# Performance work log

Hardware: AMD Instinct MI355X
Metric: run time of the kernel (lower is better)

Reference implementation:

```python
import jax, jax.numpy as jnp
import numpy as np

D_MODEL = 1024
N_HEADS = 16
HEAD_DIM = D_MODEL // N_HEADS


def setup_inputs() -> dict:
    key = jax.random.key(0)
    k_x, k_q, k_k, k_v = jax.random.split(key, 4)
    B, S = 2, 2048
    x = jax.random.normal(k_x, (B, S, D_MODEL), dtype=jnp.float32)
    # nn.Linear weights stored as [out, in]; we apply x @ W.T
    scale = 1.0 / np.sqrt(D_MODEL)
    W_q = jax.random.uniform(k_q, (D_MODEL, D_MODEL), jnp.float32, -scale, scale)
    W_k = jax.random.uniform(k_k, (D_MODEL, D_MODEL), jnp.float32, -scale, scale)
    W_v = jax.random.uniform(k_v, (D_MODEL, D_MODEL), jnp.float32, -scale, scale)
    return {"x": x, "W_q": W_q, "W_k": W_k, "W_v": W_v}


def reference(x, W_q, W_k, W_v):
    B, S, D = x.shape
    H, Hd = N_HEADS, HEAD_DIM
    # QKV projections (Linear with no bias): x @ W.T
    Q = (x @ W_q.T).reshape(B, S, H, Hd).transpose(0, 2, 1, 3)  # [B,H,S,Hd]
    K = (x @ W_k.T).reshape(B, S, H, Hd).transpose(0, 2, 1, 3)
    V = (x @ W_v.T).reshape(B, S, H, Hd).transpose(0, 2, 1, 3)
    scores = jnp.einsum("bhqd,bhkd->bhqk", Q, K) / jnp.sqrt(jnp.float32(Hd))
    attn = jax.nn.softmax(scores, axis=-1)
    out = jnp.einsum("bhqk,bhkd->bhqd", attn, V)  # [B,H,S,Hd]
    return out.transpose(0, 2, 1, 3).reshape(B, S, H * Hd)
```

## Files before the change

### kernel.cpp

```cpp
#include <hip/hip_runtime.h>
#include <stdint.h>


typedef __bf16 bf16x8 __attribute__((ext_vector_type(8)));
typedef __bf16 bf16x4 __attribute__((ext_vector_type(4)));
typedef float  f32x4  __attribute__((ext_vector_type(4)));
typedef float  f32x16 __attribute__((ext_vector_type(16)));

#define D_MODEL 1024
#define SEQ     2048
#define NHEAD   16
#define HDIM    64
#define BS      4096

__device__ __forceinline__ void load_lds16(const void* g, void* lds) {
  __builtin_amdgcn_global_load_lds(
      (__attribute__((address_space(1))) void*)(uintptr_t)g,
      (__attribute__((address_space(3))) void*)(uintptr_t)lds,
      16, 0, 0);
}

#define NX4 1048576
#define NW4 262144
__global__ void cvt_all(const float* __restrict__ x,  const float* __restrict__ wq,
                        const float* __restrict__ wk, const float* __restrict__ wv,
                        __bf16* __restrict__ xb,  __bf16* __restrict__ wqb,
                        __bf16* __restrict__ wkb, __bf16* __restrict__ wvb) {
  int i = blockIdx.x * blockDim.x + threadIdx.x;
  const float* in; __bf16* out; int j;
  if (i < NX4)                { in = x;  out = xb;  j = i; }
  else if (i < NX4 + NW4)     { in = wq; out = wqb; j = i - NX4; }
  else if (i < NX4 + 2*NW4)   { in = wk; out = wkb; j = i - NX4 - NW4; }
  else                        { in = wv; out = wvb; j = i - NX4 - 2*NW4; }
  float4 v = ((const float4*)in)[j];
  bf16x4 o;
  o[0] = (__bf16)v.x; o[1] = (__bf16)v.y;
  o[2] = (__bf16)v.z; o[3] = (__bf16)v.w;
  ((bf16x4*)out)[j] = o;
}

__global__ __launch_bounds__(256) void qkv_gemm(
    const __bf16* __restrict__ X,
    const __bf16* __restrict__ Wq, const __bf16* __restrict__ Wk,
    const __bf16* __restrict__ Wv,
    __bf16* __restrict__ Qb, __bf16* __restrict__ Kb, __bf16* __restrict__ Vt) {
  __shared__ __bf16 As[128 * 32];
  __shared__ __bf16 Bs[128 * 32];

  const __bf16* W = (blockIdx.z == 0) ? Wq : (blockIdx.z == 1) ? Wk : Wv;

  const int t    = threadIdx.x;
  const int wv   = t >> 6;
  const int lane = t & 63;
  const int l15  = lane & 15;
  const int quad = lane >> 4;
  const int m0   = blockIdx.y * 128;
  const int n0   = blockIdx.x * 128;
  const int wm   = (wv >> 1) * 64;
  const int wn   = (wv & 1) * 64;

  f32x4 acc[4][4] = {};

  for (int it = 0; it < 32; ++it) {
    const int k0 = it * 32;
#pragma unroll
    for (int p = 0; p < 2; ++p) {
      const int c   = p * 256 + t;
      const int row = c >> 2;
      const int ko  = (c & 3) * 8;
      const unsigned lb = (unsigned)((p * 256 + wv * 64) * 16);
      load_lds16(X + (size_t)(m0 + row) * D_MODEL + k0 + ko, (char*)As + lb);
      load_lds16(W + (size_t)(n0 + row) * D_MODEL + k0 + ko, (char*)Bs + lb);
    }
    __syncthreads();

    bf16x8 af[4], bfb[4];
#pragma unroll
    for (int i = 0; i < 4; ++i)
      af[i] = *(const bf16x8*)&As[(wm + i * 16 + l15) * 32 + quad * 8];
#pragma unroll
    for (int j = 0; j < 4; ++j)
      bfb[j] = *(const bf16x8*)&Bs[(wn + j * 16 + l15) * 32 + quad * 8];
#pragma unroll
    for (int i = 0; i < 4; ++i)
#pragma unroll
      for (int j = 0; j < 4; ++j)
        acc[i][j] = __builtin_amdgcn_mfma_f32_16x16x32_bf16(af[i], bfb[j],
                                                            acc[i][j], 0, 0, 0);
    __syncthreads();
  }

  if (blockIdx.z != 2) {
    __bf16* Out = (blockIdx.z == 0) ? Qb : Kb;
    const float qs = (blockIdx.z == 0) ? 0.125f : 1.0f;
#pragma unroll
    for (int i = 0; i < 4; ++i) {
      const int rg = m0 + wm + i * 16 + quad * 4;
#pragma unroll
      for (int j = 0; j < 4; ++j) {
        const int cg = n0 + wn + j * 16 + l15;
#pragma unroll
        for (int r = 0; r < 4; ++r)
          Out[(size_t)(rg + r) * D_MODEL + cg] = (__bf16)(acc[i][j][r] * qs);
      }
    }
  } else {
#pragma unroll
    for (int i = 0; i < 4; ++i) {
      const int mg = m0 + wm + i * 16 + quad * 4;
#pragma unroll
      for (int j = 0; j < 4; ++j) {
        const int ng = n0 + wn + j * 16 + l15;
        bf16x4 v;
#pragma unroll
        for (int r = 0; r < 4; ++r) v[r] = (__bf16)acc[i][j][r];
        *(bf16x4*)&Vt[(size_t)ng * BS + mg] = v;
      }
    }
  }
}

__global__ __launch_bounds__(256) void attn(
    const __bf16* __restrict__ Qb, const __bf16* __restrict__ Kb,
    const __bf16* __restrict__ Vt, float* __restrict__ out) {
  __shared__ __bf16 Ks[64 * 64];
  __shared__ __bf16 Vs[64 * 64];

  const int t    = threadIdx.x;
  const int wv   = t >> 6;
  const int lane = t & 63;
  const int l31  = lane & 31;
  const int half = lane >> 5;
  const int h    = blockIdx.y;
  const size_t bo = (size_t)blockIdx.z * SEQ;
  const int q0   = blockIdx.x * 128 + wv * 32;
  const int hd0  = h * HDIM;

  bf16x8 qf[4];
#pragma unroll
  for (int c = 0; c < 4; ++c)
    qf[c] = *(const bf16x8*)&Qb[(bo + q0 + l31) * D_MODEL + hd0 + c * 16 + half * 8];

  float lsum = 0.f;
  f32x16 o_acc[2] = {};

  for (int kt = 0; kt < SEQ / 64; ++kt) {
    const int n0 = kt * 64;
#pragma unroll
    for (int p = 0; p < 2; ++p) {
      const int c   = p * 256 + t;
      const int row = c >> 3;
      const int cc  = (c & 7) ^ (row & 7);
      const unsigned lb = (unsigned)((p * 256 + wv * 64) * 16);
      load_lds16(Kb + (bo + n0 + row) * D_MODEL + hd0 + cc * 8, (char*)Ks + lb);
      load_lds16(Vt + (size_t)(hd0 + row) * BS + bo + n0 + cc * 8, (char*)Vs + lb);
    }
    __syncthreads();

    f32x16 st[2];
#pragma unroll
    for (int ktile = 0; ktile < 2; ++ktile) {
      f32x16 acc = {};
      const int row = ktile * 32 + l31;
#pragma unroll
      for (int c = 0; c < 4; ++c) {
        const int pc = (2 * c + half) ^ (row & 7);
        bf16x8 kf = *(const bf16x8*)&Ks[(row * 8 + pc) * 8];
        acc = __builtin_amdgcn_mfma_f32_32x32x16_bf16(kf, qf[c], acc, 0, 0, 0);
      }
      st[ktile] = acc;
    }

    uint32_t pk[2][8];
#pragma unroll
    for (int ktile = 0; ktile < 2; ++ktile)
#pragma unroll
      for (int i = 0; i < 8; ++i) {
        float e0 = __expf(st[ktile][2 * i]);
        float e1 = __expf(st[ktile][2 * i + 1]);
        lsum += e0 + e1;
        union { bf16x4 v; uint32_t u[2]; } pp;
        pp.v[0] = (__bf16)e0; pp.v[1] = (__bf16)e1;
        pk[ktile][i] = pp.u[0];
      }

#pragma unroll
    for (int ktile = 0; ktile < 2; ++ktile)
#pragma unroll
      for (int kc = 0; kc < 2; ++kc) {
        auto r02 = __builtin_amdgcn_permlane32_swap(pk[ktile][kc * 4 + 0],
                                                    pk[ktile][kc * 4 + 2],
                                                    false, false);
        auto r13 = __builtin_amdgcn_permlane32_swap(pk[ktile][kc * 4 + 1],
                                                    pk[ktile][kc * 4 + 3],
                                                    false, false);
        union { uint32_t u[4]; bf16x8 v; } pf;
        pf.u[0] = r02[0]; pf.u[1] = r13[0];
        pf.u[2] = r02[1]; pf.u[3] = r13[1];
#pragma unroll
        for (int dt = 0; dt < 2; ++dt) {
          const int row = dt * 32 + l31;
          const int pc  = (ktile * 4 + kc * 2 + half) ^ (row & 7);
          bf16x8 vf = *(const bf16x8*)&Vs[(row * 8 + pc) * 8];
          o_acc[dt] = __builtin_amdgcn_mfma_f32_32x32x16_bf16(vf, pf.v,
                                                              o_acc[dt], 0, 0, 0);
        }
      }
    __syncthreads();
  }

  lsum += __shfl_xor(lsum, 32);
  const float inv = 1.f / lsum;

  const size_t orow = (bo + q0 + l31) * D_MODEL + hd0;
#pragma unroll
  for (int dt = 0; dt < 2; ++dt)
#pragma unroll
    for (int g = 0; g < 4; ++g) {
      float4 v = make_float4(o_acc[dt][4 * g + 0] * inv, o_acc[dt][4 * g + 1] * inv,
                             o_acc[dt][4 * g + 2] * inv, o_acc[dt][4 * g + 3] * inv);
      *(float4*)&out[orow + dt * 32 + g * 8 + half * 4] = v;
    }
}

extern "C" void kernel_launch(void* const* d_in, const int* in_sizes, int n_in,
                              void* d_out, int out_size, void* d_ws, size_t ws_size,
                              hipStream_t stream) {
  const float* x  = (const float*)d_in[0];
  const float* Wq = (const float*)d_in[1];
  const float* Wk = (const float*)d_in[2];
  const float* Wv = (const float*)d_in[3];
  float* out = (float*)d_out;

  char* ws = (char*)d_ws;
  __bf16* xb  = (__bf16*)(ws);
  __bf16* wqb = (__bf16*)(ws + (8u  << 20));
  __bf16* wkb = (__bf16*)(ws + (10u << 20));
  __bf16* wvb = (__bf16*)(ws + (12u << 20));
  __bf16* Qbf = (__bf16*)(ws + (14u << 20));
  __bf16* Kbf = (__bf16*)(ws + (22u << 20));
  __bf16* Vt  = (__bf16*)(ws + (30u << 20));

  cvt_all<<<(NX4 + 3 * NW4) / 256, 256, 0, stream>>>(x, Wq, Wk, Wv,
                                                     xb, wqb, wkb, wvb);

  qkv_gemm<<<dim3(8, 32, 3), 256, 0, stream>>>(xb, wqb, wkb, wvb, Qbf, Kbf, Vt);

  attn<<<dim3(SEQ / 128, NHEAD, 2), 256, 0, stream>>>(Qbf, Kbf, Vt, out);
}
```

Measured before the change: 168.5 us.

## Double-buffer LDS tiles with register prefetch in QKV GEMM and attention

Replaces direct global-to-LDS loads with a register-staged prefetch: the next tile's global loads are issued right after the barrier, then written to the alternate LDS buffer at the top of the next iteration. This removes one __syncthreads per iteration and lets global-load latency overlap with the MFMA work in both kernels. The cost is doubled LDS use, extra VGPRs for the staged data, and a VGPR-to-LDS write round trip in place of the async direct load.

```diff
diff --git a/kernel.cpp b/kernel.cpp
--- a/kernel.cpp
+++ b/kernel.cpp
@@ -12,13 +12,6 @@
 #define NHEAD   16
 #define HDIM    64
 #define BS      4096
-
-__device__ __forceinline__ void load_lds16(const void* g, void* lds) {
-  __builtin_amdgcn_global_load_lds(
-      (__attribute__((address_space(1))) void*)(uintptr_t)g,
-      (__attribute__((address_space(3))) void*)(uintptr_t)lds,
-      16, 0, 0);
-}
 
 #define NX4 1048576
 #define NW4 262144
@@ -44,8 +37,8 @@
     const __bf16* __restrict__ Wq, const __bf16* __restrict__ Wk,
     const __bf16* __restrict__ Wv,
     __bf16* __restrict__ Qb, __bf16* __restrict__ Kb, __bf16* __restrict__ Vt) {
-  __shared__ __bf16 As[128 * 32];
-  __shared__ __bf16 Bs[128 * 32];
+  __shared__ __bf16 As[2][128 * 32];
+  __shared__ __bf16 Bs[2][128 * 32];
 
   const __bf16* W = (blockIdx.z == 0) ? Wq : (blockIdx.z == 1) ? Wk : Wv;
 
@@ -59,35 +52,47 @@
   const int wm   = (wv >> 1) * 64;
   const int wn   = (wv & 1) * 64;
 
+  const int c0 = t, c1 = 256 + t;
+  const int ar0 = c0 >> 2, ak0 = (c0 & 3) * 8;
+  const int ar1 = c1 >> 2, ak1 = (c1 & 3) * 8;
+
+  uint4 r[4];
+  auto glead = [&](int k0) {
+    r[0] = *(const uint4*)(X + (size_t)(m0 + ar0) * D_MODEL + k0 + ak0);
+    r[1] = *(const uint4*)(X + (size_t)(m0 + ar1) * D_MODEL + k0 + ak1);
+    r[2] = *(const uint4*)(W + (size_t)(n0 + ar0) * D_MODEL + k0 + ak0);
+    r[3] = *(const uint4*)(W + (size_t)(n0 + ar1) * D_MODEL + k0 + ak1);
+  };
+  auto lwrite = [&](int b) {
+    *(uint4*)((char*)As[b] + c0 * 16) = r[0];
+    *(uint4*)((char*)As[b] + c1 * 16) = r[1];
+    *(uint4*)((char*)Bs[b] + c0 * 16) = r[2];
+    *(uint4*)((char*)Bs[b] + c1 * 16) = r[3];
+  };
+
   f32x4 acc[4][4] = {};
 
+  glead(0);
+#pragma unroll 1
   for (int it = 0; it < 32; ++it) {
-    const int k0 = it * 32;
-#pragma unroll
-    for (int p = 0; p < 2; ++p) {
-      const int c   = p * 256 + t;
-      const int row = c >> 2;
-      const int ko  = (c & 3) * 8;
-      const unsigned lb = (unsigned)((p * 256 + wv * 64) * 16);
-      load_lds16(X + (size_t)(m0 + row) * D_MODEL + k0 + ko, (char*)As + lb);
-      load_lds16(W + (size_t)(n0 + row) * D_MODEL + k0 + ko, (char*)Bs + lb);
-    }
+    const int b = it & 1;
+    lwrite(b);
     __syncthreads();
+    if (it + 1 < 32) glead((it + 1) * 32);
 
     bf16x8 af[4], bfb[4];
 #pragma unroll
     for (int i = 0; i < 4; ++i)
-      af[i] = *(const bf16x8*)&As[(wm + i * 16 + l15) * 32 + quad * 8];
+      af[i] = *(const bf16x8*)&As[b][(wm + i * 16 + l15) * 32 + quad * 8];
 #pragma unroll
     for (int j = 0; j < 4; ++j)
-      bfb[j] = *(const bf16x8*)&Bs[(wn + j * 16 + l15) * 32 + quad * 8];
+      bfb[j] = *(const bf16x8*)&Bs[b][(wn + j * 16 + l15) * 32 + quad * 8];
 #pragma unroll
     for (int i = 0; i < 4; ++i)
 #pragma unroll
       for (int j = 0; j < 4; ++j)
         acc[i][j] = __builtin_amdgcn_mfma_f32_16x16x32_bf16(af[i], bfb[j],
                                                             acc[i][j], 0, 0, 0);
-    __syncthreads();
   }
 
   if (blockIdx.z != 2) {
@@ -100,8 +105,8 @@
       for (int j = 0; j < 4; ++j) {
         const int cg = n0 + wn + j * 16 + l15;
 #pragma unroll
-        for (int r = 0; r < 4; ++r)
-          Out[(size_t)(rg + r) * D_MODEL + cg] = (__bf16)(acc[i][j][r] * qs);
+        for (int r2 = 0; r2 < 4; ++r2)
+          Out[(size_t)(rg + r2) * D_MODEL + cg] = (__bf16)(acc[i][j][r2] * qs);
       }
     }
   } else {
@@ -113,7 +118,7 @@
         const int ng = n0 + wn + j * 16 + l15;
         bf16x4 v;
 #pragma unroll
-        for (int r = 0; r < 4; ++r) v[r] = (__bf16)acc[i][j][r];
+        for (int r2 = 0; r2 < 4; ++r2) v[r2] = (__bf16)acc[i][j][r2];
         *(bf16x4*)&Vt[(size_t)ng * BS + mg] = v;
       }
     }
@@ -123,17 +128,16 @@
 __global__ __launch_bounds__(256) void attn(
     const __bf16* __restrict__ Qb, const __bf16* __restrict__ Kb,
     const __bf16* __restrict__ Vt, float* __restrict__ out) {
-  __shared__ __bf16 Ks[64 * 64];
-  __shared__ __bf16 Vs[64 * 64];
+  __shared__ __bf16 Ks[2][64 * 64];
+  __shared__ __bf16 Vs[2][64 * 64];
 
   const int t    = threadIdx.x;
-  const int wv   = t >> 6;
   const int lane = t & 63;
   const int l31  = lane & 31;
   const int half = lane >> 5;
   const int h    = blockIdx.y;
   const size_t bo = (size_t)blockIdx.z * SEQ;
-  const int q0   = blockIdx.x * 128 + wv * 32;
+  const int q0   = blockIdx.x * 128 + (t >> 6) * 32;
   const int hd0  = h * HDIM;
 
   bf16x8 qf[4];
@@ -144,18 +148,34 @@
   float lsum = 0.f;
   f32x16 o_acc[2] = {};
 
+  const int c0 = t, c1 = 256 + t;
+  const int row0 = c0 >> 3, cc0 = (c0 & 7) ^ (row0 & 7);
+  const int row1 = c1 >> 3, cc1 = (c1 & 7) ^ (row1 & 7);
+
+  uint4 r[4];
+  auto glead = [&](int n0) {
+    r[0] = *(const uint4*)(Kb + (bo + n0 + row0) * D_MODEL + hd0 + cc0 * 8);
+    r[1] = *(const uint4*)(Kb + (bo + n0 + row1) * D_MODEL + hd0 + cc1 * 8);
+    r[2] = *(const uint4*)(Vt + (size_t)(hd0 + row0) * BS + bo + n0 + cc0 * 8);
+    r[3] = *(const uint4*)(Vt + (size_t)(hd0 + row1) * BS + bo + n0 + cc1 * 8);
+  };
+  auto lwrite = [&](int b) {
+    *(uint4*)((char*)Ks[b] + c0 * 16) = r[0];
+    *(uint4*)((char*)Ks[b] + c1 * 16) = r[1];
+    *(uint4*)((char*)Vs[b] + c0 * 16) = r[2];
+    *(uint4*)((char*)Vs[b] + c1 * 16) = r[3];
+  };
+
+  glead(0);
+#pragma unroll 1
   for (int kt = 0; kt < SEQ / 64; ++kt) {
-    const int n0 = kt * 64;
-#pragma unroll
-    for (int p = 0; p < 2; ++p) {
-      const int c   = p * 256 + t;
-      const int row = c >> 3;
-      const int cc  = (c & 7) ^ (row & 7);
-      const unsigned lb = (unsigned)((p * 256 + wv * 64) * 16);
-      load_lds16(Kb + (bo + n0 + row) * D_MODEL + hd0 + cc * 8, (char*)Ks + lb);
-      load_lds16(Vt + (size_t)(hd0 + row) * BS + bo + n0 + cc * 8, (char*)Vs + lb);
-    }
+    const int b = kt & 1;
+    lwrite(b);
     __syncthreads();
+    if (kt + 1 < SEQ / 64) glead((kt + 1) * 64);
+
+    const __bf16* ks = Ks[b];
+    const __bf16* vs = Vs[b];
 
     f32x16 st[2];
 #pragma unroll
@@ -165,7 +185,7 @@
 #pragma unroll
       for (int c = 0; c < 4; ++c) {
         const int pc = (2 * c + half) ^ (row & 7);
-        bf16x8 kf = *(const bf16x8*)&Ks[(row * 8 + pc) * 8];
+        bf16x8 kf = *(const bf16x8*)&ks[(row * 8 + pc) * 8];
         acc = __builtin_amdgcn_mfma_f32_32x32x16_bf16(kf, qf[c], acc, 0, 0, 0);
       }
       st[ktile] = acc;
@@ -201,12 +221,11 @@
         for (int dt = 0; dt < 2; ++dt) {
           const int row = dt * 32 + l31;
           const int pc  = (ktile * 4 + kc * 2 + half) ^ (row & 7);
-          bf16x8 vf = *(const bf16x8*)&Vs[(row * 8 + pc) * 8];
+          bf16x8 vf = *(const bf16x8*)&vs[(row * 8 + pc) * 8];
           o_acc[dt] = __builtin_amdgcn_mfma_f32_32x32x16_bf16(vf, pf.v,
                                                               o_acc[dt], 0, 0, 0);
         }
       }
-    __syncthreads();
   }
 
   lsum += __shfl_xor(lsum, 32);
```

Result: slower. 278.3 us (+65.2%).
